# Performance work log

Hardware: AMD Instinct MI355X
Metric: run time of the kernel (lower is better)

Reference implementation:

```python
import jax, jax.numpy as jnp
import numpy as np

N_NODES = 50000
C = 128
E = 800000
B = 4096
NEG = 5
NUM_LAYERS = 3


def setup_inputs() -> dict:
    key = jax.random.key(0)
    ks = jax.random.split(key, 8)
    edge_index = jax.random.randint(ks[0], (2, E), 0, N_NODES, dtype=jnp.int64)
    edge_weight = jax.random.uniform(ks[1], (E,), dtype=jnp.float32)
    n_id = jax.random.randint(ks[2], ((2 + NEG) * B,), 0, N_NODES, dtype=jnp.int64)
    x = jnp.zeros((1,), jnp.float32)  # ignored by forward (overwritten by id_embed)
    id_embed = jax.random.normal(ks[3], (N_NODES, C), jnp.float32) * 0.1
    w1 = jax.random.normal(ks[4], (2 * C, C), jnp.float32) * (1.0 / np.sqrt(2 * C))
    b1 = jnp.zeros((C,), jnp.float32)
    w2 = jax.random.normal(ks[5], (C, 1), jnp.float32) * (1.0 / np.sqrt(C))
    b2 = jnp.zeros((1,), jnp.float32)
    return {"x": x, "edge_index": edge_index, "edge_weight": edge_weight,
            "n_id": n_id, "neg_sample_num": NEG, "id_embed": id_embed,
            "w1": w1, "b1": b1, "w2": w2, "b2": b2}


def reference(x, edge_index, edge_weight, n_id, neg_sample_num, id_embed, w1, b1, w2, b2):
    n_nodes = id_embed.shape[0]
    row, col = edge_index[0], edge_index[1]
    # symmetric GCN normalization (LGCConv)
    deg = jax.ops.segment_sum(jnp.ones_like(row, dtype=id_embed.dtype), row,
                              num_segments=n_nodes)
    dinv = jnp.where(deg > 0, jax.lax.rsqrt(jnp.maximum(deg, 1e-12)), 0.0)
    norm = (dinv[row] * dinv[col])[:, None]  # [E,1]
    h = id_embed
    final = id_embed
    for _ in range(NUM_LAYERS):
        h = jax.ops.segment_sum(norm * h[col], row, num_segments=n_nodes)
        final = final + h
    final = final / (NUM_LAYERS + 1)
    # split n_id into (out, pos, neg) index groups
    b = n_id.shape[0] // (2 + neg_sample_num)
    out = final[n_id[:b]]
    pos = final[n_id[b:2 * b]]
    neg = final[n_id[2 * b:]]
    tiled_out = jnp.repeat(out, neg_sample_num, axis=0)  # [b*neg, C]

    def pred_head(z):  # Linear -> LeakyReLU(0.2) -> (Dropout eval=identity) -> Linear
        z = jax.nn.leaky_relu(z @ w1 + b1, negative_slope=0.2)
        return z @ w2 + b2

    pos_logit = pred_head(jnp.concatenate([out, pos], axis=-1))
    neg_logits = pred_head(jnp.concatenate([tiled_out, neg], axis=-1))
    return pos_logit, neg_logits
```

## Files before the change

### kernel.cpp

```cpp
#include <hip/hip_runtime.h>
#include <hip/hip_bf16.h>

#define C 128
#define NBKT 128
#define BCAP 8192

typedef __bf16 bf16x8 __attribute__((ext_vector_type(8)));
typedef float floatx4 __attribute__((ext_vector_type(4)));

__device__ __forceinline__ unsigned short f2bf(float f) {
    unsigned u = __float_as_uint(f);
    unsigned r = (u + 0x7FFFu + ((u >> 16) & 1u)) >> 16;
    return (unsigned short)r;
}
__device__ __forceinline__ float bflo(unsigned v) { return __uint_as_float(v << 16); }
__device__ __forceinline__ float bfhi(unsigned v) { return __uint_as_float(v & 0xFFFF0000u); }
__device__ __forceinline__ unsigned packbf(float lo, float hi) {
    return (unsigned)f2bf(lo) | ((unsigned)f2bf(hi) << 16);
}

__device__ __forceinline__ int g_idx(const void* p, long long i, int is64) {
    if (is64) return (int)((const long long*)p)[i];
    return ((const int*)p)[i];
}
__device__ __forceinline__ float g_flt(const void* p, long long i, int isf32) {
    if (isf32) return ((const float*)p)[i];
    return __uint_as_float(((unsigned)((const unsigned short*)p)[i]) << 16);
}

__global__ void k_detect(const void* edge, const void* nid, const void* emb, int* flags,
                         unsigned* g0, unsigned* g1, unsigned* g2, int* bucketcnt,
                         int N, int SST) {
    int t = threadIdx.x;
    int buf = t >> 6, w = t & 63;
    size_t o = (size_t)(w >> 5) * SST + (size_t)N * 32 + (w & 31);
    if (buf == 0) g0[o] = 0;
    else if (buf == 1) g1[o] = 0;
    else g2[o] = 0;
    if (t < NBKT) bucketcnt[t] = 0;
    if (t < 64) {
        const unsigned* wrd = (const unsigned*)edge;
        const unsigned* nw = (const unsigned*)nid;
        int predA = (t < 32) ? (wrd[2 * t + 1] == 0u) : 1;
        int predB = (t < 32) ? (nw[2 * t + 1] == 0u) : 1;
        const unsigned short* h = (const unsigned short*)emb;
        int ex = (h[2 * t] >> 7) & 0xFF;
        int plaus = (ex >= 0x6C && ex <= 0x7F) ? 1 : 0;
        unsigned long long mA = __ballot(predA);
        unsigned long long mB = __ballot(predB);
        unsigned long long mP = __ballot(plaus);
        if (t == 0) {
            flags[0] = (mA == ~0ull) ? 1 : 0;
            flags[1] = (mB == ~0ull) ? 1 : 0;
            flags[2] = (__popcll(mP) < 32) ? 1 : 0;
        }
    }
}

__global__ void k_bucketA(const void* edge, int E, int rpb, const int* flags,
                          unsigned* __restrict__ bucketbuf, int* __restrict__ bucketcnt) {
    __shared__ int lcnt[NBKT];
    __shared__ int lbase[NBKT];
    int t = threadIdx.x;
    int is64 = flags[0];
    const int PER = 8;
    int chunkSz = blockDim.x * PER;
    long long stride = (long long)gridDim.x * chunkSz;
    for (long long base = (long long)blockIdx.x * chunkSz; base < E; base += stride) {
        if (t < NBKT) lcnt[t] = 0;
        __syncthreads();
        int bkt[PER], rank[PER];
        unsigned enc[PER];
        long long e0 = base + (long long)t * PER;
        int rr[PER], cc[PER];
        if (e0 + PER <= E) {
            if (is64) {
                const long long* pr = (const long long*)edge + e0;
                const long long* pc = (const long long*)edge + E + e0;
#pragma unroll
                for (int j = 0; j < PER; j += 2) {
                    longlong2 vr = *(const longlong2*)(pr + j);
                    longlong2 vc = *(const longlong2*)(pc + j);
                    rr[j] = (int)vr.x; rr[j + 1] = (int)vr.y;
                    cc[j] = (int)vc.x; cc[j + 1] = (int)vc.y;
                }
            } else {
                const int* pr = (const int*)edge + e0;
                const int* pc = (const int*)edge + E + e0;
#pragma unroll
                for (int j = 0; j < PER; j += 4) {
                    int4 vr = *(const int4*)(pr + j);
                    int4 vc = *(const int4*)(pc + j);
                    rr[j] = vr.x; rr[j + 1] = vr.y; rr[j + 2] = vr.z; rr[j + 3] = vr.w;
                    cc[j] = vc.x; cc[j + 1] = vc.y; cc[j + 2] = vc.z; cc[j + 3] = vc.w;
                }
            }
#pragma unroll
            for (int j = 0; j < PER; ++j) {
                int b = rr[j] / rpb;
                bkt[j] = b;
                enc[j] = ((unsigned)(rr[j] - b * rpb) << 16) | (unsigned)(cc[j] & 0xFFFF);
                rank[j] = atomicAdd(&lcnt[b], 1);
            }
        } else {
#pragma unroll
            for (int j = 0; j < PER; ++j) {
                long long e = e0 + j;
                if (e < E) {
                    int r = g_idx(edge, e, is64);
                    int c = g_idx(edge, (long long)E + e, is64);
                    int b = r / rpb;
                    bkt[j] = b;
                    enc[j] = ((unsigned)(r - b * rpb) << 16) | (unsigned)(c & 0xFFFF);
                    rank[j] = atomicAdd(&lcnt[b], 1);
                } else bkt[j] = -1;
            }
        }
        __syncthreads();
        if (t < NBKT) lbase[t] = atomicAdd(&bucketcnt[t], lcnt[t]);
        __syncthreads();
#pragma unroll
        for (int j = 0; j < PER; ++j) {
            if (bkt[j] >= 0) {
                int pos = lbase[bkt[j]] + rank[j];
                if (pos < BCAP)
                    bucketbuf[(size_t)bkt[j] * BCAP + pos] = enc[j];
            }
        }
    }
}

__global__ __launch_bounds__(512) void k_bsort(
        const unsigned* __restrict__ bucketbuf, const int* __restrict__ bucketcnt,
        int* __restrict__ rowptr, float* __restrict__ dinv, float* __restrict__ di2,
        float* __restrict__ rdinv, unsigned short* __restrict__ cols16, int N, int rpb) {
    __shared__ int hist[512];
    int b = blockIdx.x;
    int t = threadIdx.x;
    int base = 0, cnt = 0, total = 0;
    for (int i = 0; i < NBKT; ++i) {
        int v = bucketcnt[i];
        if (v > BCAP) v = BCAP;
        if (i < b) base += v;
        if (i == b) cnt = v;
        total += v;
    }
    int r0 = b * rpb;
    int rows = N - r0;
    if (rows > rpb) rows = rpb;
    if (rows < 0) rows = 0;

    hist[t] = 0;
    __syncthreads();
    const unsigned* buf = bucketbuf + (size_t)b * BCAP;
    for (int i = t; i < cnt; i += 512) atomicAdd(&hist[buf[i] >> 16], 1);
    __syncthreads();
    int v = hist[t];
    __syncthreads();
    for (int off = 1; off < 512; off <<= 1) {
        int x = (t >= off) ? hist[t - off] : 0;
        __syncthreads();
        hist[t] += x;
        __syncthreads();
    }
    int excl = hist[t] - v;
    if (t < rows) {
        int r = r0 + t;
        rowptr[r] = base + excl;
        float fd = (float)v;
        float dv = (v > 0) ? rsqrtf(fd) : 0.0f;
        dinv[r] = dv;
        di2[r] = dv * dv;
        rdinv[r] = (v > 0) ? sqrtf(fd) : 0.0f;
    }
    if (b == NBKT - 1 && t == 0) rowptr[N] = total;
    __syncthreads();
    hist[t] = base + excl;
    __syncthreads();
    for (int i = t; i < cnt; i += 512) {
        unsigned u = buf[i];
        int pos = atomicAdd(&hist[u >> 16], 1);
        cols16[pos] = (unsigned short)(u & 0xFFFF);
    }
}

__global__ void k_initprep(const void* emb, const float* __restrict__ dinv,
                           unsigned* __restrict__ h0, unsigned* __restrict__ g0,
                           int n2, int SST,
                           const void* w1, const void* b1, const void* w2, const void* b2,
                           unsigned short* __restrict__ w1t, float* __restrict__ b1f,
                           float* __restrict__ w2f, float* __restrict__ b2f, const int* flags) {
    int i = blockIdx.x * blockDim.x + threadIdx.x;
    int f32 = flags[2];
    if (i < n2) {
        float lo = g_flt(emb, 2LL * i, f32);
        float hi = g_flt(emb, 2LL * i + 1, f32);
        int n = i >> 6, w = i & 63;
        size_t o = (size_t)(w >> 5) * SST + (size_t)n * 32 + (w & 31);
        h0[o] = packbf(lo, hi);
        float dv = dinv[n];
        g0[o] = packbf(lo * dv, hi * dv);
    }
    if (i < 256 * 128) {
        int k = i >> 7, n = i & 127;
        w1t[n * 256 + k] = f2bf(g_flt(w1, i, f32));
    }
    if (i < 128) {
        b1f[i] = g_flt(b1, i, f32);
        w2f[i] = g_flt(w2, i, f32);
    }
    if (i == 0) b2f[0] = g_flt(b2, 0, f32);
}

__global__ void k_layer(const int* __restrict__ rowptr, const unsigned short* __restrict__ cols16,
                        const uint4* __restrict__ gin, uint4* __restrict__ gout,
                        const float* __restrict__ di2, int N, int SSTU4) {
    int slice = blockIdx.x & 1;
    int node = (blockIdx.x >> 1) * 32 + (threadIdx.x >> 3);
    if (node >= N) return;
    int l8 = threadIdx.x & 7;
    const uint4* gs = gin + (size_t)slice * SSTU4;
    int p = rowptr[node];
    int end = rowptr[node + 1];
    float a0 = 0.f, a1 = 0.f, a2 = 0.f, a3 = 0.f;
    float a4 = 0.f, a5 = 0.f, a6 = 0.f, a7 = 0.f;
    for (int base = p; base < end; base += 8) {
        int c[8];
#pragma unroll
        for (int j = 0; j < 8; ++j) {
            int idx = base + j;
            int cv = cols16[idx];
            c[j] = (idx < end) ? cv : N;
        }
#pragma unroll
        for (int j = 0; j < 8; ++j) {
            uint4 v = gs[(size_t)c[j] * 8 + l8];
            a0 += bflo(v.x); a1 += bfhi(v.x);
            a2 += bflo(v.y); a3 += bfhi(v.y);
            a4 += bflo(v.z); a5 += bfhi(v.z);
            a6 += bflo(v.w); a7 += bfhi(v.w);
        }
    }
    float s = di2[node];
    uint4 o;
    o.x = packbf(a0 * s, a1 * s);
    o.y = packbf(a2 * s, a3 * s);
    o.z = packbf(a4 * s, a5 * s);
    o.w = packbf(a6 * s, a7 * s);
    gout[(size_t)slice * SSTU4 + (size_t)node * 8 + l8] = o;
}

__global__ void k_layer3(const int* __restrict__ rowptr, const unsigned short* __restrict__ cols16,
                         const uint4* __restrict__ gin , const uint4* __restrict__ h0,
                         const uint4* __restrict__ g1, uint4* __restrict__ fin,
                         const float* __restrict__ di2, const float* __restrict__ rdinv,
                         int N, int SSTU4) {
    int slice = blockIdx.x & 1;
    int node = (blockIdx.x >> 1) * 32 + (threadIdx.x >> 3);
    if (node >= N) return;
    int l8 = threadIdx.x & 7;
    size_t sb = (size_t)slice * SSTU4;
    const uint4* gs = gin + sb;
    int p = rowptr[node];
    int end = rowptr[node + 1];
    float a0 = 0.f, a1 = 0.f, a2 = 0.f, a3 = 0.f;
    float a4 = 0.f, a5 = 0.f, a6 = 0.f, a7 = 0.f;
    for (int base = p; base < end; base += 8) {
        int c[8];
#pragma unroll
        for (int j = 0; j < 8; ++j) {
            int idx = base + j;
            int cv = cols16[idx];
            c[j] = (idx < end) ? cv : N;
        }
#pragma unroll
        for (int j = 0; j < 8; ++j) {
            uint4 v = gs[(size_t)c[j] * 8 + l8];
            a0 += bflo(v.x); a1 += bfhi(v.x);
            a2 += bflo(v.y); a3 += bfhi(v.y);
            a4 += bflo(v.z); a5 += bfhi(v.z);
            a6 += bflo(v.w); a7 += bfhi(v.w);
        }
    }
    float s = di2[node];
    float rd = rdinv[node];
    size_t ro = (size_t)node * 8 + l8;
    uint4 x0 = h0[sb + ro];
    uint4 x1 = g1[sb + ro];
    uint4 x2 = gs[ro];
    uint4 o;
    o.x = packbf(0.25f * (bflo(x0.x) + rd * (bflo(x1.x) + bflo(x2.x) + s * a0)),
                 0.25f * (bfhi(x0.x) + rd * (bfhi(x1.x) + bfhi(x2.x) + s * a1)));
    o.y = packbf(0.25f * (bflo(x0.y) + rd * (bflo(x1.y) + bflo(x2.y) + s * a2)),
                 0.25f * (bfhi(x0.y) + rd * (bfhi(x1.y) + bfhi(x2.y) + s * a3)));
    o.z = packbf(0.25f * (bflo(x0.z) + rd * (bflo(x1.z) + bflo(x2.z) + s * a4)),
                 0.25f * (bfhi(x0.z) + rd * (bfhi(x1.z) + bfhi(x2.z) + s * a5)));
    o.w = packbf(0.25f * (bflo(x0.w) + rd * (bflo(x1.w) + bflo(x2.w) + s * a6)),
                 0.25f * (bfhi(x0.w) + rd * (bfhi(x1.w) + bfhi(x2.w) + s * a7)));
    fin[(size_t)node * 16 + slice * 8 + l8] = o;
}

__global__ void k_head(const uint4* __restrict__ fin, const void* n_id,
                       const unsigned short* __restrict__ w1t,
                       const float* __restrict__ b1f, const float* __restrict__ w2f,
                       const float* __restrict__ b2f,
                       float* __restrict__ out, int B, int NEG, const int* flags) {
    __shared__ unsigned short z[64][264];
    int t = threadIdx.x;
    int id64 = flags[1];
    int mbase = blockIdx.x * 64;

#pragma unroll
    for (int i = 0; i < 8; ++i) {
        int flat = i * 256 + t;
        int m = flat >> 5;
        int q = flat & 31;
        int gm = mbase + m;
        int r;
        if (gm < B) {
            r = (q < 16) ? g_idx(n_id, gm, id64) : g_idx(n_id, B + gm, id64);
        } else {
            int j = gm - B;
            r = (q < 16) ? g_idx(n_id, j / NEG, id64) : g_idx(n_id, 2 * B + j, id64);
        }
        uint4 v = fin[(size_t)r * 16 + (q & 15)];
        *(uint4*)((char*)&z[m][0] + q * 16) = v;
    }
    __syncthreads();

    int wave = t >> 6, lane = t & 63;
    int quad = lane >> 4, l16 = lane & 15;

    floatx4 acc[8] = {};
    bf16x8 a[8];
    const unsigned short* zrow = &z[wave * 16 + l16][0];
#pragma unroll
    for (int ks = 0; ks < 8; ++ks)
        a[ks] = *(const bf16x8*)(zrow + ks * 32 + quad * 8);

#pragma unroll
    for (int ks = 0; ks < 8; ++ks) {
#pragma unroll
        for (int nt = 0; nt < 8; ++nt) {
            bf16x8 b = *(const bf16x8*)(w1t + (nt * 16 + l16) * 256 + ks * 32 + quad * 8);
            acc[nt] = __builtin_amdgcn_mfma_f32_16x16x32_bf16(a[ks], b, acc[nt], 0, 0, 0);
        }
    }

    float s0 = 0.f, s1 = 0.f, s2 = 0.f, s3 = 0.f;
#pragma unroll
    for (int nt = 0; nt < 8; ++nt) {
        int col = nt * 16 + l16;
        float bb = b1f[col], ww = w2f[col];
        float v0 = acc[nt][0] + bb; v0 = (v0 > 0.f) ? v0 : 0.2f * v0; s0 += v0 * ww;
        float v1 = acc[nt][1] + bb; v1 = (v1 > 0.f) ? v1 : 0.2f * v1; s1 += v1 * ww;
        float v2 = acc[nt][2] + bb; v2 = (v2 > 0.f) ? v2 : 0.2f * v2; s2 += v2 * ww;
        float v3 = acc[nt][3] + bb; v3 = (v3 > 0.f) ? v3 : 0.2f * v3; s3 += v3 * ww;
    }
#pragma unroll
    for (int off = 1; off <= 8; off <<= 1) {
        s0 += __shfl_xor(s0, off, 64);
        s1 += __shfl_xor(s1, off, 64);
        s2 += __shfl_xor(s2, off, 64);
        s3 += __shfl_xor(s3, off, 64);
    }
    if (l16 == 0) {
        int rowbase = mbase + wave * 16 + quad * 4;
        float bb2 = b2f[0];
        out[rowbase + 0] = s0 + bb2;
        out[rowbase + 1] = s1 + bb2;
        out[rowbase + 2] = s2 + bb2;
        out[rowbase + 3] = s3 + bb2;
    }
}

extern "C" void kernel_launch(void* const* d_in, const int* in_sizes, int n_in,
                              void* d_out, int out_size, void* d_ws, size_t ws_size,
                              hipStream_t stream) {
    const void* edge_index = d_in[1];
    const void* n_id       = d_in[3];
    const void* id_embed   = d_in[5];
    const void* w1 = d_in[6];
    const void* b1 = d_in[7];
    const void* w2 = d_in[8];
    const void* b2 = d_in[9];
    float* out = (float*)d_out;

    const int E  = in_sizes[1] / 2;
    const int N  = in_sizes[5] / C;
    const int NEG = 5;
    const int B  = in_sizes[3] / (2 + NEG);
    const int n_out_rows = B + B * NEG;
    const int SST = (N + 1) * 32;
    const int SSTU4 = (N + 1) * 8;
    const int NB = 2 * SST;
    const int rpb = (N + NBKT - 1) / NBKT;

    size_t off = 0;
    auto alloc = [&](size_t nf) {
        char* p = (char*)d_ws + off * 4;
        off += (nf + 255) & ~(size_t)255;
        return p;
    };
    int*   flags     = (int*)alloc(8);
    int*   bucketcnt = (int*)alloc(NBKT);
    float* dinv      = (float*)alloc(N);
    float* di2       = (float*)alloc(N);
    float* rdinv     = (float*)alloc(N);
    int*   rowptr    = (int*)alloc(N + 1);
    unsigned short* cols16 = (unsigned short*)alloc(((size_t)E + 16 + 1) / 2);
    unsigned* bucketbuf = (unsigned*)alloc((size_t)NBKT * BCAP);
    unsigned* h0     = (unsigned*)alloc(NB);
    unsigned* g0     = (unsigned*)alloc(NB);
    unsigned* g1     = (unsigned*)alloc(NB);
    unsigned* g2     = (unsigned*)alloc(NB);
    unsigned* fin    = (unsigned*)alloc((size_t)N * 64);
    unsigned short* w1t = (unsigned short*)alloc(256 * 128 / 2);
    float* b1f       = (float*)alloc(C);
    float* w2f       = (float*)alloc(C);
    float* b2f       = (float*)alloc(8);

    const int BS = 256;
    k_detect<<<1, 192, 0, stream>>>(edge_index, n_id, id_embed, flags, g0, g1, g2,
                                    bucketcnt, N, SST);
    const int gridA = (E + BS * 8 - 1) / (BS * 8);
    k_bucketA<<<gridA, BS, 0, stream>>>(edge_index, E, rpb, flags, bucketbuf, bucketcnt);
    k_bsort<<<NBKT, 512, 0, stream>>>(bucketbuf, bucketcnt, rowptr, dinv, di2, rdinv,
                                      cols16, N, rpb);
    k_initprep<<<(N * 64 + BS - 1) / BS, BS, 0, stream>>>(
        id_embed, dinv, h0, g0, N * 64, SST, w1, b1, w2, b2, w1t, b1f, w2f, b2f, flags);

    const int layer_grid = ((N + 31) / 32) * 2;
    k_layer<<<layer_grid, BS, 0, stream>>>(rowptr, cols16, (const uint4*)g0, (uint4*)g1,
                                           di2, N, SSTU4);
    k_layer<<<layer_grid, BS, 0, stream>>>(rowptr, cols16, (const uint4*)g1, (uint4*)g2,
                                           di2, N, SSTU4);
    k_layer3<<<layer_grid, BS, 0, stream>>>(rowptr, cols16, (const uint4*)g2, (const uint4*)h0,
                                            (const uint4*)g1, (uint4*)fin, di2, rdinv,
                                            N, SSTU4);

    k_head<<<n_out_rows / 64, BS, 0, stream>>>((const uint4*)fin, n_id, w1t, b1f, w2f, b2f,
                                               out, B, NEG, flags);
}
```

Measured before the change: 217.0 us.

## Reorder nodes by degree class to balance work in SpMM layer kernels

Nodes are binned into 16 classes by degree (deg>>3) during the bucket sort, and a permutation grouping nodes of similar degree is built in the init kernel. The layer kernels then process nodes in permuted order, so the 8-lane groups in a wavefront run similar numbers of loop iterations and idle less from divergence. The cost is an extra indirection per node, scattered output writes, and some extra atomics and a serial prefix in every init block.

```diff
diff --git a/kernel.cpp b/kernel.cpp
--- a/kernel.cpp
+++ b/kernel.cpp
@@ -30,7 +30,7 @@
 
 __global__ void k_detect(const void* edge, const void* nid, const void* emb, int* flags,
                          unsigned* g0, unsigned* g1, unsigned* g2, int* bucketcnt,
-                         int N, int SST) {
+                         int* clscnt, int N, int SST) {
     int t = threadIdx.x;
     int buf = t >> 6, w = t & 63;
     size_t o = (size_t)(w >> 5) * SST + (size_t)N * 32 + (w & 31);
@@ -38,6 +38,7 @@
     else if (buf == 1) g1[o] = 0;
     else g2[o] = 0;
     if (t < NBKT) bucketcnt[t] = 0;
+    if (t < 16) clscnt[t] = 0;
     if (t < 64) {
         const unsigned* wrd = (const unsigned*)edge;
         const unsigned* nw = (const unsigned*)nid;
@@ -133,8 +134,11 @@
 __global__ __launch_bounds__(512) void k_bsort(
         const unsigned* __restrict__ bucketbuf, const int* __restrict__ bucketcnt,
         int* __restrict__ rowptr, float* __restrict__ dinv, float* __restrict__ di2,
-        float* __restrict__ rdinv, unsigned short* __restrict__ cols16, int N, int rpb) {
+        float* __restrict__ rdinv, unsigned short* __restrict__ cols16,
+        int* __restrict__ nodecls, int* __restrict__ clscnt, int N, int rpb) {
     __shared__ int hist[512];
+    __shared__ int chist[16];
+    __shared__ int cbase[16];
     int b = blockIdx.x;
     int t = threadIdx.x;
     int base = 0, cnt = 0, total = 0;
@@ -151,6 +155,7 @@
     if (rows < 0) rows = 0;
 
     hist[t] = 0;
+    if (t < 16) chist[t] = 0;
     __syncthreads();
     const unsigned* buf = bucketbuf + (size_t)b * BCAP;
     for (int i = t; i < cnt; i += 512) atomicAdd(&hist[buf[i] >> 16], 1);
@@ -175,8 +180,17 @@
     }
     if (b == NBKT - 1 && t == 0) rowptr[N] = total;
     __syncthreads();
+    int cls = 0, lrank = 0;
+    if (t < rows) {
+        cls = v >> 3;
+        if (cls > 15) cls = 15;
+        lrank = atomicAdd(&chist[cls], 1);
+    }
     hist[t] = base + excl;
     __syncthreads();
+    if (t < 16) cbase[t] = atomicAdd(&clscnt[t], chist[t]);
+    __syncthreads();
+    if (t < rows) nodecls[r0 + t] = (cls << 20) | (cbase[cls] + lrank);
     for (int i = t; i < cnt; i += 512) {
         unsigned u = buf[i];
         int pos = atomicAdd(&hist[u >> 16], 1);
@@ -189,7 +203,15 @@
                            int n2, int SST,
                            const void* w1, const void* b1, const void* w2, const void* b2,
                            unsigned short* __restrict__ w1t, float* __restrict__ b1f,
-                           float* __restrict__ w2f, float* __restrict__ b2f, const int* flags) {
+                           float* __restrict__ w2f, float* __restrict__ b2f,
+                           const int* __restrict__ nodecls, const int* __restrict__ clscnt,
+                           int* __restrict__ perm, int N, const int* flags) {
+    __shared__ int clsoff[16];
+    if (threadIdx.x == 0) {
+        int s = 0;
+        for (int k2 = 0; k2 < 16; ++k2) { clsoff[k2] = s; s += clscnt[k2]; }
+    }
+    __syncthreads();
     int i = blockIdx.x * blockDim.x + threadIdx.x;
     int f32 = flags[2];
     if (i < n2) {
@@ -201,6 +223,10 @@
         float dv = dinv[n];
         g0[o] = packbf(lo * dv, hi * dv);
     }
+    if (i < N) {
+        int v = nodecls[i];
+        perm[clsoff[v >> 20] + (v & 0xFFFFF)] = i;
+    }
     if (i < 256 * 128) {
         int k = i >> 7, n = i & 127;
         w1t[n * 256 + k] = f2bf(g_flt(w1, i, f32));
@@ -214,10 +240,12 @@
 
 __global__ void k_layer(const int* __restrict__ rowptr, const unsigned short* __restrict__ cols16,
                         const uint4* __restrict__ gin, uint4* __restrict__ gout,
-                        const float* __restrict__ di2, int N, int SSTU4) {
+                        const float* __restrict__ di2, const int* __restrict__ perm,
+                        int N, int SSTU4) {
     int slice = blockIdx.x & 1;
-    int node = (blockIdx.x >> 1) * 32 + (threadIdx.x >> 3);
-    if (node >= N) return;
+    int nidx = (blockIdx.x >> 1) * 32 + (threadIdx.x >> 3);
+    if (nidx >= N) return;
+    int node = perm[nidx];
     int l8 = threadIdx.x & 7;
     const uint4* gs = gin + (size_t)slice * SSTU4;
     int p = rowptr[node];
@@ -254,10 +282,11 @@
                          const uint4* __restrict__ gin , const uint4* __restrict__ h0,
                          const uint4* __restrict__ g1, uint4* __restrict__ fin,
                          const float* __restrict__ di2, const float* __restrict__ rdinv,
-                         int N, int SSTU4) {
+                         const int* __restrict__ perm, int N, int SSTU4) {
     int slice = blockIdx.x & 1;
-    int node = (blockIdx.x >> 1) * 32 + (threadIdx.x >> 3);
-    if (node >= N) return;
+    int nidx = (blockIdx.x >> 1) * 32 + (threadIdx.x >> 3);
+    if (nidx >= N) return;
+    int node = perm[nidx];
     int l8 = threadIdx.x & 7;
     size_t sb = (size_t)slice * SSTU4;
     const uint4* gs = gin + sb;
@@ -404,10 +433,13 @@
     };
     int*   flags     = (int*)alloc(8);
     int*   bucketcnt = (int*)alloc(NBKT);
+    int*   clscnt    = (int*)alloc(16);
     float* dinv      = (float*)alloc(N);
     float* di2       = (float*)alloc(N);
     float* rdinv     = (float*)alloc(N);
     int*   rowptr    = (int*)alloc(N + 1);
+    int*   nodecls   = (int*)alloc(N);
+    int*   perm      = (int*)alloc(N);
     unsigned short* cols16 = (unsigned short*)alloc(((size_t)E + 16 + 1) / 2);
     unsigned* bucketbuf = (unsigned*)alloc((size_t)NBKT * BCAP);
     unsigned* h0     = (unsigned*)alloc(NB);
@@ -422,22 +454,23 @@
 
     const int BS = 256;
     k_detect<<<1, 192, 0, stream>>>(edge_index, n_id, id_embed, flags, g0, g1, g2,
-                                    bucketcnt, N, SST);
+                                    bucketcnt, clscnt, N, SST);
     const int gridA = (E + BS * 8 - 1) / (BS * 8);
     k_bucketA<<<gridA, BS, 0, stream>>>(edge_index, E, rpb, flags, bucketbuf, bucketcnt);
     k_bsort<<<NBKT, 512, 0, stream>>>(bucketbuf, bucketcnt, rowptr, dinv, di2, rdinv,
-                                      cols16, N, rpb);
+                                      cols16, nodecls, clscnt, N, rpb);
     k_initprep<<<(N * 64 + BS - 1) / BS, BS, 0, stream>>>(
-        id_embed, dinv, h0, g0, N * 64, SST, w1, b1, w2, b2, w1t, b1f, w2f, b2f, flags);
+        id_embed, dinv, h0, g0, N * 64, SST, w1, b1, w2, b2, w1t, b1f, w2f, b2f,
+        nodecls, clscnt, perm, N, flags);
 
     const int layer_grid = ((N + 31) / 32) * 2;
     k_layer<<<layer_grid, BS, 0, stream>>>(rowptr, cols16, (const uint4*)g0, (uint4*)g1,
-                                           di2, N, SSTU4);
+                                           di2, perm, N, SSTU4);
     k_layer<<<layer_grid, BS, 0, stream>>>(rowptr, cols16, (const uint4*)g1, (uint4*)g2,
-                                           di2, N, SSTU4);
+                                           di2, perm, N, SSTU4);
     k_layer3<<<layer_grid, BS, 0, stream>>>(rowptr, cols16, (const uint4*)g2, (const uint4*)h0,
                                             (const uint4*)g1, (uint4*)fin, di2, rdinv,
-                                            N, SSTU4);
+                                            perm, N, SSTU4);
 
     k_head<<<n_out_rows / 64, BS, 0, stream>>>((const uint4*)fin, n_id, w1t, b1f, w2f, b2f,
                                                out, B, NEG, flags);
```

Measured after the change: 221.8 us. +2.2%, slower.
